# Optimization experiments

Hardware: AMD Instinct MI355X
Metric: run time of the kernel (lower is better)

## Reference

```python
import jax, jax.numpy as jnp
import numpy as np

VOCAB, EMBED, HIDDEN, LAYERS = 256, 256, 1024, 2
B, T = 128, 256


def gru_layer(x_seq, h0, W_ih, W_hh, b_ih, b_hh):
    """PyTorch-semantics GRU layer. x_seq:[B,T,in], h0:[B,H] -> ([B,T,H], [B,H]).
    n = tanh(W_in x + b_in + r * (W_hn h + b_hn)); h' = (1-z)*n + z*h.
    Input-gate GEMM is hoisted out of the scan (one big matmul over all T)."""
    H = h0.shape[-1]
    gi = jnp.einsum('bti,gi->btg', x_seq, W_ih) + b_ih  # [B,T,3H]
    gi = jnp.transpose(gi, (1, 0, 2))                   # [T,B,3H] scan over time

    def step(h, gi_t):
        gh = h @ W_hh.T + b_hh                          # [B,3H]
        i_r, i_z, i_n = jnp.split(gi_t, 3, axis=-1)
        h_r, h_z, h_n = jnp.split(gh, 3, axis=-1)
        r = jax.nn.sigmoid(i_r + h_r)
        z = jax.nn.sigmoid(i_z + h_z)
        n = jnp.tanh(i_n + r * h_n)
        h_new = (1.0 - z) * n + z * h
        return h_new, h_new

    h_last, ys = jax.lax.scan(step, h0, gi)
    return jnp.transpose(ys, (1, 0, 2)), h_last         # [B,T,H], [B,H]


def setup_inputs() -> dict:
    key = jax.random.key(0)
    ks = jax.random.split(key, 16)
    s = 1.0 / np.sqrt(HIDDEN)
    u = lambda k, shape: jax.random.uniform(k, shape, jnp.float32, -s, s)
    inp = {
        'x': jax.random.randint(ks[0], (B, T), 0, VOCAB),
        'h0': jax.random.normal(ks[1], (LAYERS, B, HIDDEN), jnp.float32),
        'emb': jax.random.normal(ks[2], (VOCAB, EMBED), jnp.float32),
        'W_ih0': u(ks[3], (3 * HIDDEN, EMBED)),
        'W_hh0': u(ks[4], (3 * HIDDEN, HIDDEN)),
        'b_ih0': u(ks[5], (3 * HIDDEN,)),
        'b_hh0': u(ks[6], (3 * HIDDEN,)),
        'W_ih1': u(ks[7], (3 * HIDDEN, HIDDEN)),
        'W_hh1': u(ks[8], (3 * HIDDEN, HIDDEN)),
        'b_ih1': u(ks[9], (3 * HIDDEN,)),
        'b_hh1': u(ks[10], (3 * HIDDEN,)),
        'fc_W': u(ks[11], (VOCAB, HIDDEN)),
        'fc_b': u(ks[12], (VOCAB,)),
    }
    return inp


def reference(x, h0, emb, W_ih0, W_hh0, b_ih0, b_hh0, W_ih1, W_hh1, b_ih1, b_hh1, fc_W, fc_b):
    xe = emb[x]                                          # [B,T,E]
    y0, h_last0 = gru_layer(xe, h0[0], W_ih0, W_hh0, b_ih0, b_hh0)
    y1, h_last1 = gru_layer(y0, h0[1], W_ih1, W_hh1, b_ih1, b_hh1)
    logits = y1[:, -1, :] @ fc_W.T + fc_b                # [B,VOCAB]
    h = jnp.stack([h_last0, h_last1], axis=0)            # [LAYERS,B,H]
    return logits, h
```

## Files before the change

kernel.cpp:

```cpp
#include <hip/hip_runtime.h>
#include <hip/hip_bf16.h>

using bf16x8 = __attribute__((ext_vector_type(8))) __bf16;
using short8 = __attribute__((ext_vector_type(8))) short;
using f32x4  = __attribute__((ext_vector_type(4))) float;
using f4     = __attribute__((ext_vector_type(4))) float;
using i32x4  = __attribute__((ext_vector_type(4))) int;

constexpr int NB = 128;
constexpr int NT = 256;
constexpr int NH = 1024;
constexpr int NE = 256;
constexpr int NV = 256;

constexpr int WHH_BYTES = 48 * 2048;
constexpr int GH_FLOATS = 24 * 256;
constexpr int NBLK = 256;

__device__ __forceinline__ void ldg_sc(i32x4& d, const void* p) {
  asm volatile("global_load_dwordx4 %0, %1, off sc0 sc1" : "=v"(d) : "v"(p));
}
__device__ __forceinline__ void stg_sc(void* p, i32x4 v) {
  asm volatile("global_store_dwordx4 %0, %1, off sc0 sc1" :: "v"(p), "v"(v) : "memory");
}
__device__ __forceinline__ void vm0_fence() {
  asm volatile("s_waitcnt vmcnt(0)" ::: "memory");
}
__device__ __forceinline__ void use_dep(i32x4& d) {
  asm volatile("" : "+v"(d));
}

__device__ __forceinline__ bf16x8 cvt8(const float* p) {
  short8 r;
  #pragma unroll
  for (int j = 0; j < 8; ++j)
    r[j] = (short)__bfloat16_as_ushort(__float2bfloat16(p[j]));
  return __builtin_bit_cast(bf16x8, r);
}

__global__ __launch_bounds__(256) void embcvt_kernel(const float* __restrict__ e,
                                                     __hip_bfloat16* __restrict__ o) {
  int i = blockIdx.x * 256 + threadIdx.x;
  o[i] = __float2bfloat16(e[i]);
}

template<int LAYER>
__global__ __launch_bounds__(384) void gru_kernel(
    const int* __restrict__ x,
    const __hip_bfloat16* __restrict__ embb,
    const float* __restrict__ Wih,
    const float* __restrict__ Whh,
    const float* __restrict__ bih,
    const float* __restrict__ bhh,
    const float* __restrict__ h0,
    const __hip_bfloat16* __restrict__ yin,
    __hip_bfloat16* __restrict__ yout,
    __hip_bfloat16* __restrict__ hbuf,
    float* __restrict__ hout,
    unsigned int* __restrict__ flags)
{
  extern __shared__ char smem[];
  char*  sWhh  = smem;
  float* sGh   = (float*)(smem + WHH_BYTES);
  float* sBias = sGh + GH_FLOATS;
  char*  sH    = (char*)(sBias + 64);

  const int tid  = threadIdx.x;
  const int lane = tid & 63;
  const int wv   = tid >> 6;
  const int mt   = wv & 1;
  const int ks   = wv >> 1;
  const int b    = blockIdx.x;
  const int rb   = (b >> 1) & 3;
  const int cidx = (b & 1) * 32 + (b >> 3);
  const int r0   = rb * 32;
  const int c0   = cidx * 16;
  unsigned int* pf = flags + rb * 64 * 16;
  const int slot = cidx;
  const int l16  = lane & 15;
  const int lk8  = (lane >> 4) * 8;

  for (int it = 0; it < 16; ++it) {
    int idx = it * 384 + tid;
    int gr = idx >> 7, kc = idx & 127;
    int grow = (gr >> 4) * NH + c0 + (gr & 15);
    short8 v = __builtin_bit_cast(short8, cvt8(Whh + grow * NH + kc * 8));
    *(short8*)(sWhh + ((gr * 2048 + kc * 16) ^ ((gr & 7) << 4))) = v;
  }
  if (tid < 16)       sBias[tid] = bih[c0 + tid] + bhh[c0 + tid];
  else if (tid < 32)  { int c = NH + c0 + tid - 16;   sBias[tid] = bih[c] + bhh[c]; }
  else if (tid < 48)  { int c = 2*NH + c0 + tid - 32; sBias[tid] = bih[c]; }
  else if (tid < 64)  { int c = 2*NH + c0 + tid - 48; sBias[tid] = bhh[c]; }

  constexpr int NFRAG = (LAYER == 0) ? 8 : 32;
  constexpr int KIN   = (LAYER == 0) ? NE : NH;
  bf16x8 wreg[NFRAG];
  #pragma unroll
  for (int kf = 0; kf < NFRAG; ++kf) {
    int grow = ks * NH + c0 + l16;
    wreg[kf] = cvt8(Wih + grow * KIN + kf * 32 + lk8);
  }

  float hown[2] = {0.f, 0.f};
  #pragma unroll
  for (int ei = 0; ei < 2; ++ei) {
    int e = tid + ei * 384;
    if (e < 512) {
      float hv = h0[(r0 + (e >> 4)) * NH + c0 + (e & 15)];
      hown[ei] = hv;
      ((unsigned short*)sH)[e] = __bfloat16_as_ushort(__float2bfloat16(hv));
    }
  }
  __syncthreads();
  if (tid < 64) {
    i32x4 hv = *(const i32x4*)(sH + (tid >> 1) * 32 + (tid & 1) * 16);
    stg_sc(hbuf + (r0 + (tid >> 1)) * NH + c0 + (tid & 1) * 8, hv);
    vm0_fence();
    if (tid == 0)
      __hip_atomic_store(pf + slot * 16, 1u, __ATOMIC_RELAXED,
                         __HIP_MEMORY_SCOPE_AGENT);
  }

  for (int t = 0; t < NT; ++t) {
    const __hip_bfloat16* rbuf = hbuf + (t & 1) * (NB * NH);
    __hip_bfloat16* wbuf = hbuf + ((t + 1) & 1) * (NB * NH);
    const int arow = r0 + mt * 16 + l16;
    const int bxor = (l16 & 7) << 4;
    float* abase = sGh + (lane >> 4) * 64 + l16;

    constexpr int P1 = (LAYER == 0) ? 4 : 24;
    f32x4 ai = {0.f, 0.f, 0.f, 0.f};
    const __hip_bfloat16* xptr;
    if constexpr (LAYER == 0) {
      int xid = x[arow * NT + t];
      xptr = embb + xid * NE + lk8;
    } else {
      xptr = yin + (arow * NT + t) * NH + lk8;
    }
    #pragma unroll
    for (int kk = 0; kk < P1; ++kk) {
      bf16x8 a = __builtin_bit_cast(bf16x8, *(const short8*)(xptr + kk * 32));
      ai = __builtin_amdgcn_mfma_f32_16x16x32_bf16(a, wreg[kk], ai, 0, 0, 0);
    }

    {
      unsigned int ep = (unsigned int)(t + 1);
      if (tid < 64) {
        const unsigned int* f = pf + tid * 16;
        while (__hip_atomic_load(f, __ATOMIC_RELAXED,
                                 __HIP_MEMORY_SCOPE_AGENT) < ep)
          __builtin_amdgcn_s_sleep(1);
      }
      __syncthreads();
    }

    const int nk = (ks < 2) ? 11 : 10;
    const __hip_bfloat16* aptr = rbuf + arow * NH + lk8;
    i32x4 fr[11];
    #pragma unroll
    for (int i = 0; i < 11; ++i)
      if (i < nk) ldg_sc(fr[i], aptr + (ks + 3 * i) * 32);

    #pragma unroll
    for (int kk = P1; kk < NFRAG; ++kk) {
      bf16x8 a = __builtin_bit_cast(bf16x8, *(const short8*)(xptr + kk * 32));
      ai = __builtin_amdgcn_mfma_f32_16x16x32_bf16(a, wreg[kk], ai, 0, 0, 0);
    }
    {
      float* p = abase + (18 + mt * 3 + ks) * 256;
      p[0] = ai[0]; p[16] = ai[1]; p[32] = ai[2]; p[48] = ai[3];
    }

    vm0_fence();
    #pragma unroll
    for (int i = 0; i < 11; ++i)
      if (i < nk) use_dep(fr[i]);
    {
      f32x4 ah0 = {0.f,0.f,0.f,0.f}, ah1 = {0.f,0.f,0.f,0.f}, ah2 = {0.f,0.f,0.f,0.f};
      const int bb0 = (l16)      * 2048 + lk8 * 2;
      const int bb1 = (16 + l16) * 2048 + lk8 * 2;
      const int bb2 = (32 + l16) * 2048 + lk8 * 2;
      #pragma unroll
      for (int i = 0; i < 11; ++i) {
        if (i < nk) {
          int kk = ks + 3 * i;
          bf16x8 a = __builtin_bit_cast(bf16x8, fr[i]);
          bf16x8 b0 = __builtin_bit_cast(bf16x8,
              *(const short8*)(sWhh + ((bb0 + kk * 64) ^ bxor)));
          ah0 = __builtin_amdgcn_mfma_f32_16x16x32_bf16(a, b0, ah0, 0, 0, 0);
          bf16x8 b1 = __builtin_bit_cast(bf16x8,
              *(const short8*)(sWhh + ((bb1 + kk * 64) ^ bxor)));
          ah1 = __builtin_amdgcn_mfma_f32_16x16x32_bf16(a, b1, ah1, 0, 0, 0);
          bf16x8 b2 = __builtin_bit_cast(bf16x8,
              *(const short8*)(sWhh + ((bb2 + kk * 64) ^ bxor)));
          ah2 = __builtin_amdgcn_mfma_f32_16x16x32_bf16(a, b2, ah2, 0, 0, 0);
        }
      }
      float* p0 = abase + (ks * 6 + mt * 3 + 0) * 256;
      float* p1 = abase + (ks * 6 + mt * 3 + 1) * 256;
      float* p2 = abase + (ks * 6 + mt * 3 + 2) * 256;
      p0[0] = ah0[0]; p0[16] = ah0[1]; p0[32] = ah0[2]; p0[48] = ah0[3];
      p1[0] = ah1[0]; p1[16] = ah1[1]; p1[32] = ah1[2]; p1[48] = ah1[3];
      p2[0] = ah2[0]; p2[16] = ah2[1]; p2[32] = ah2[2]; p2[48] = ah2[3];
    }
    __syncthreads();

    #pragma unroll
    for (int ei = 0; ei < 2; ++ei) {
      int e = tid + ei * 384;
      if (e < 512) {
        int lrow = e >> 4, lcol = e & 15;
        int m2 = lrow >> 4, off = (lrow & 15) * 16 + lcol;
        float ghr = sGh[(0*6 + m2*3 + 0) * 256 + off]
                  + sGh[(1*6 + m2*3 + 0) * 256 + off]
                  + sGh[(2*6 + m2*3 + 0) * 256 + off];
        float ghz = sGh[(0*6 + m2*3 + 1) * 256 + off]
                  + sGh[(1*6 + m2*3 + 1) * 256 + off]
                  + sGh[(2*6 + m2*3 + 1) * 256 + off];
        float ghn = sGh[(0*6 + m2*3 + 2) * 256 + off]
                  + sGh[(1*6 + m2*3 + 2) * 256 + off]
                  + sGh[(2*6 + m2*3 + 2) * 256 + off];
        float gir = sGh[(18 + m2*3 + 0) * 256 + off];
        float giz = sGh[(18 + m2*3 + 1) * 256 + off];
        float gin = sGh[(18 + m2*3 + 2) * 256 + off];
        float r = 1.f / (1.f + __expf(-(gir + ghr + sBias[lcol])));
        float z = 1.f / (1.f + __expf(-(giz + ghz + sBias[16 + lcol])));
        float npre = (gin + sBias[32 + lcol]) + r * (ghn + sBias[48 + lcol]);
        float n = 2.f / (1.f + __expf(-2.f * npre)) - 1.f;
        float hn = (1.f - z) * n + z * hown[ei];
        hown[ei] = hn;
        __hip_bfloat16 hb = __float2bfloat16(hn);
        ((unsigned short*)sH)[e] = __bfloat16_as_ushort(hb);
        if constexpr (LAYER == 0)
          yout[((r0 + lrow) * NT + t) * NH + c0 + lcol] = hb;
      }
    }

    __syncthreads();
    if (tid < 64) {
      i32x4 hv = *(const i32x4*)(sH + (tid >> 1) * 32 + (tid & 1) * 16);
      stg_sc(wbuf + (r0 + (tid >> 1)) * NH + c0 + (tid & 1) * 8, hv);
      vm0_fence();
      if (tid == 0)
        __hip_atomic_store(pf + slot * 16, (unsigned int)(t + 2),
                           __ATOMIC_RELAXED, __HIP_MEMORY_SCOPE_AGENT);
    }
  }

  #pragma unroll
  for (int ei = 0; ei < 2; ++ei) {
    int e = tid + ei * 384;
    if (e < 512) {
      int lrow = e >> 4, lcol = e & 15;
      hout[(r0 + lrow) * NH + c0 + lcol] = hown[ei];
    }
  }
}

__global__ __launch_bounds__(256) void logits_kernel(
    const __hip_bfloat16* __restrict__ h1,
    const float* __restrict__ fcW,
    const float* __restrict__ fcb,
    float* __restrict__ out)
{
  __shared__ float hrow[NH];
  int b = blockIdx.x, v = threadIdx.x;
  if (v < 128) {
    i32x4 hv;
    ldg_sc(hv, h1 + b * NH + v * 8);
    vm0_fence();
    use_dep(hv);
    short8 s = __builtin_bit_cast(short8, hv);
    #pragma unroll
    for (int j = 0; j < 8; ++j) {
      union { unsigned int i; float f; } c;
      c.i = ((unsigned int)(unsigned short)s[j]) << 16;
      hrow[v * 8 + j] = c.f;
    }
  }
  __syncthreads();
  float acc = fcb[v];
  for (int k = 0; k < NH; k += 4) {
    f4 wv = *(const f4*)(fcW + v * NH + k);
    #pragma unroll
    for (int j = 0; j < 4; ++j) acc += wv[j] * hrow[k + j];
  }
  out[b * NV + v] = acc;
}

extern "C" void kernel_launch(void* const* d_in, const int* in_sizes, int n_in,
                              void* d_out, int out_size, void* d_ws, size_t ws_size,
                              hipStream_t stream) {
  const int*   x    = (const int*)d_in[0];
  const float* h0   = (const float*)d_in[1];
  const float* emb  = (const float*)d_in[2];
  const float* Wih0 = (const float*)d_in[3];
  const float* Whh0 = (const float*)d_in[4];
  const float* bih0 = (const float*)d_in[5];
  const float* bhh0 = (const float*)d_in[6];
  const float* Wih1 = (const float*)d_in[7];
  const float* Whh1 = (const float*)d_in[8];
  const float* bih1 = (const float*)d_in[9];
  const float* bhh1 = (const float*)d_in[10];
  const float* fcW  = (const float*)d_in[11];
  const float* fcb  = (const float*)d_in[12];
  float* out = (float*)d_out;

  char* ws = (char*)d_ws;
  size_t off = 0;
  __hip_bfloat16* y0   = (__hip_bfloat16*)ws;            off += (size_t)NB * NT * NH * 2;
  __hip_bfloat16* hbuf = (__hip_bfloat16*)(ws + off);    off += (size_t)2 * NB * NH * 2;
  __hip_bfloat16* embb = (__hip_bfloat16*)(ws + off);    off += (size_t)NV * NE * 2;
  unsigned int*  flags0 = (unsigned int*)(ws + off);     off += 4 * 64 * 16 * 4;
  unsigned int*  flags1 = (unsigned int*)(ws + off);     off += 4 * 64 * 16 * 4;

  (void)hipMemsetAsync(flags0, 0, 2 * 4 * 64 * 16 * 4, stream);
  embcvt_kernel<<<dim3(NV * NE / 256), dim3(256), 0, stream>>>(emb, embb);

  constexpr int lds = WHH_BYTES + GH_FLOATS * 4 + 64 * 4 + 1024;
  (void)hipFuncSetAttribute(reinterpret_cast<const void*>(gru_kernel<0>),
                            hipFuncAttributeMaxDynamicSharedMemorySize, lds);
  (void)hipFuncSetAttribute(reinterpret_cast<const void*>(gru_kernel<1>),
                            hipFuncAttributeMaxDynamicSharedMemorySize, lds);

  gru_kernel<0><<<dim3(NBLK), dim3(384), lds, stream>>>(
      x, embb, Wih0, Whh0, bih0, bhh0, h0, y0, y0, hbuf, out + 32768, flags0);
  gru_kernel<1><<<dim3(NBLK), dim3(384), lds, stream>>>(
      x, embb, Wih1, Whh1, bih1, bhh1, h0 + NB * NH, y0, y0, hbuf,
      out + 32768 + NB * NH, flags1);
  logits_kernel<<<dim3(NB), dim3(256), 0, stream>>>(hbuf, fcW, fcb, out);
}
```

Before: 4.082 ms.

## Fuse both GRU layers into one wavefront-pipelined persistent kernel

```diff
diff --git a/kernel.cpp b/kernel.cpp
--- a/kernel.cpp
+++ b/kernel.cpp
@@ -12,10 +12,11 @@
 constexpr int NH = 1024;
 constexpr int NE = 256;
 constexpr int NV = 256;
+constexpr int BH = NB * NH;
 
 constexpr int WHH_BYTES = 48 * 2048;
-constexpr int GH_FLOATS = 24 * 256;
-constexpr int NBLK = 256;
+constexpr int NTILE     = 60;
+constexpr int GH_FLOATS = NTILE * 256;
 
 __device__ __forceinline__ void ldg_sc(i32x4& d, const void* p) {
   asm volatile("global_load_dwordx4 %0, %1, off sc0 sc1" : "=v"(d) : "v"(p));
@@ -44,18 +45,16 @@
   o[i] = __float2bfloat16(e[i]);
 }
 
-template<int LAYER>
-__global__ __launch_bounds__(384) void gru_kernel(
+__global__ __launch_bounds__(384, 2) void gru_fused(
     const int* __restrict__ x,
     const __hip_bfloat16* __restrict__ embb,
-    const float* __restrict__ Wih,
-    const float* __restrict__ Whh,
-    const float* __restrict__ bih,
-    const float* __restrict__ bhh,
+    const float* __restrict__ Wih0, const float* __restrict__ Whh0,
+    const float* __restrict__ bih0, const float* __restrict__ bhh0,
+    const float* __restrict__ Wih1, const float* __restrict__ Whh1,
+    const float* __restrict__ bih1, const float* __restrict__ bhh1,
     const float* __restrict__ h0,
-    const __hip_bfloat16* __restrict__ yin,
-    __hip_bfloat16* __restrict__ yout,
-    __hip_bfloat16* __restrict__ hbuf,
+    __hip_bfloat16* __restrict__ Ys,
+    __hip_bfloat16* __restrict__ hbuf1,
     float* __restrict__ hout,
     unsigned int* __restrict__ flags)
 {
@@ -65,24 +64,33 @@
   float* sBias = sGh + GH_FLOATS;
   char*  sH    = (char*)(sBias + 64);
 
-  const int tid  = threadIdx.x;
-  const int lane = tid & 63;
-  const int wv   = tid >> 6;
-  const int mt   = wv & 1;
-  const int ks   = wv >> 1;
-  const int b    = blockIdx.x;
-  const int rb   = (b >> 1) & 3;
-  const int cidx = (b & 1) * 32 + (b >> 3);
-  const int r0   = rb * 32;
-  const int c0   = cidx * 16;
-  unsigned int* pf = flags + rb * 64 * 16;
-  const int slot = cidx;
-  const int l16  = lane & 15;
-  const int lk8  = (lane >> 4) * 8;
+  const int tid   = threadIdx.x;
+  const int lane  = tid & 63;
+  const int wv    = tid >> 6;
+  const int mt    = wv & 1;
+  const int ks    = wv >> 1;
+  const int b     = blockIdx.x;
+  const int layer = b & 1;
+  const int idx   = b >> 1;
+  const int rb2   = idx & 1;
+  const int cidx  = idx >> 1;
+  const int r0    = rb2 * 64;
+  const int c0    = cidx * 16;
+  unsigned int* flagL  = flags + (layer * 2 + rb2) * 64 * 16;
+  unsigned int* flag0g = flags + (rb2) * 64 * 16;
+  const int l16 = lane & 15;
+  const int lk8 = (lane >> 4) * 8;
+
+  const float* Wih = layer ? Wih1 : Wih0;
+  const float* Whh = layer ? Whh1 : Whh0;
+  const float* bih = layer ? bih1 : bih0;
+  const float* bhh = layer ? bhh1 : bhh0;
+  const float* h0l = h0 + layer * BH;
+  float* houtl = hout + layer * BH;
 
   for (int it = 0; it < 16; ++it) {
-    int idx = it * 384 + tid;
-    int gr = idx >> 7, kc = idx & 127;
+    int id2 = it * 384 + tid;
+    int gr = id2 >> 7, kc = id2 & 127;
     int grow = (gr >> 4) * NH + c0 + (gr & 15);
     short8 v = __builtin_bit_cast(short8, cvt8(Whh + grow * NH + kc * 8));
     *(short8*)(sWhh + ((gr * 2048 + kc * 16) ^ ((gr & 7) << 4))) = v;
@@ -92,167 +100,261 @@
   else if (tid < 48)  { int c = 2*NH + c0 + tid - 32; sBias[tid] = bih[c]; }
   else if (tid < 64)  { int c = 2*NH + c0 + tid - 48; sBias[tid] = bhh[c]; }
 
-  constexpr int NFRAG = (LAYER == 0) ? 8 : 32;
-  constexpr int KIN   = (LAYER == 0) ? NE : NH;
-  bf16x8 wreg[NFRAG];
+  bf16x8 wreg[16];
+  if (layer == 0) {
+    #pragma unroll
+    for (int kf = 0; kf < 4; ++kf)
+      wreg[kf] = cvt8(Wih + (ks * NH + c0 + l16) * NE + mt * 128 + kf * 32 + lk8);
+  } else {
+    #pragma unroll
+    for (int kf = 0; kf < 16; ++kf)
+      wreg[kf] = cvt8(Wih + (ks * NH + c0 + l16) * NH + mt * 512 + kf * 32 + lk8);
+  }
+
+  float hown[3] = {0.f, 0.f, 0.f};
   #pragma unroll
-  for (int kf = 0; kf < NFRAG; ++kf) {
-    int grow = ks * NH + c0 + l16;
-    wreg[kf] = cvt8(Wih + grow * KIN + kf * 32 + lk8);
-  }
-
-  float hown[2] = {0.f, 0.f};
-  #pragma unroll
-  for (int ei = 0; ei < 2; ++ei) {
+  for (int ei = 0; ei < 3; ++ei) {
     int e = tid + ei * 384;
-    if (e < 512) {
-      float hv = h0[(r0 + (e >> 4)) * NH + c0 + (e & 15)];
+    if (e < 1024) {
+      int row = e >> 4, col = e & 15;
+      float hv = h0l[(r0 + row) * NH + c0 + col];
       hown[ei] = hv;
       ((unsigned short*)sH)[e] = __bfloat16_as_ushort(__float2bfloat16(hv));
     }
   }
   __syncthreads();
-  if (tid < 64) {
-    i32x4 hv = *(const i32x4*)(sH + (tid >> 1) * 32 + (tid & 1) * 16);
-    stg_sc(hbuf + (r0 + (tid >> 1)) * NH + c0 + (tid & 1) * 8, hv);
+  if (layer == 1) {
+    if (tid < 128) {
+      i32x4 hv = *(const i32x4*)(sH + (tid >> 1) * 32 + (tid & 1) * 16);
+      stg_sc(hbuf1 + (r0 + (tid >> 1)) * NH + c0 + (tid & 1) * 8, hv);
+    }
     vm0_fence();
     if (tid == 0)
-      __hip_atomic_store(pf + slot * 16, 1u, __ATOMIC_RELAXED,
+      __hip_atomic_store(flagL + cidx * 16, 1u, __ATOMIC_RELAXED,
                          __HIP_MEMORY_SCOPE_AGENT);
-  }
-
-  for (int t = 0; t < NT; ++t) {
-    const __hip_bfloat16* rbuf = hbuf + (t & 1) * (NB * NH);
-    __hip_bfloat16* wbuf = hbuf + ((t + 1) & 1) * (NB * NH);
-    const int arow = r0 + mt * 16 + l16;
-    const int bxor = (l16 & 7) << 4;
-    float* abase = sGh + (lane >> 4) * 64 + l16;
-
-    constexpr int P1 = (LAYER == 0) ? 4 : 24;
-    f32x4 ai = {0.f, 0.f, 0.f, 0.f};
-    const __hip_bfloat16* xptr;
-    if constexpr (LAYER == 0) {
-      int xid = x[arow * NT + t];
-      xptr = embb + xid * NE + lk8;
-    } else {
-      xptr = yin + (arow * NT + t) * NH + lk8;
-    }
-    #pragma unroll
-    for (int kk = 0; kk < P1; ++kk) {
-      bf16x8 a = __builtin_bit_cast(bf16x8, *(const short8*)(xptr + kk * 32));
-      ai = __builtin_amdgcn_mfma_f32_16x16x32_bf16(a, wreg[kk], ai, 0, 0, 0);
-    }
-
-    {
-      unsigned int ep = (unsigned int)(t + 1);
-      if (tid < 64) {
-        const unsigned int* f = pf + tid * 16;
+    __builtin_amdgcn_fence(__ATOMIC_ACQUIRE, "agent");
+  }
+
+  const int bxor = (l16 & 7) << 4;
+  float* abase = sGh + (lane >> 4) * 64 + l16;
+  const int nk = (ks < 2) ? 11 : 10;
+  const int bb0 = (l16)      * 2048 + lk8 * 2;
+  const int bb1 = (16 + l16) * 2048 + lk8 * 2;
+  const int bb2 = (32 + l16) * 2048 + lk8 * 2;
+
+  if (layer == 0) {
+    for (int t = 0; t < NT; ++t) {
+      #pragma unroll
+      for (int m4 = 0; m4 < 4; ++m4) {
+        int xid = x[(r0 + m4 * 16 + l16) * NT + t];
+        const __hip_bfloat16* xp = embb + xid * NE + mt * 128 + lk8;
+        f32x4 ii = {0.f, 0.f, 0.f, 0.f};
+        #pragma unroll
+        for (int kf = 0; kf < 4; ++kf) {
+          bf16x8 a = __builtin_bit_cast(bf16x8, *(const short8*)(xp + kf * 32));
+          ii = __builtin_amdgcn_mfma_f32_16x16x32_bf16(a, wreg[kf], ii, 0, 0, 0);
+        }
+        float* p = abase + (36 + (ks * 2 + mt) * 4 + m4) * 256;
+        p[0] = ii[0]; p[16] = ii[1]; p[32] = ii[2]; p[48] = ii[3];
+      }
+      if (t > 0 && tid < 64) {
+        unsigned int ep = (unsigned int)(t + 1);
+        const unsigned int* f = flagL + tid * 16;
         while (__hip_atomic_load(f, __ATOMIC_RELAXED,
                                  __HIP_MEMORY_SCOPE_AGENT) < ep)
           __builtin_amdgcn_s_sleep(1);
       }
       __syncthreads();
-    }
-
-    const int nk = (ks < 2) ? 11 : 10;
-    const __hip_bfloat16* aptr = rbuf + arow * NH + lk8;
-    i32x4 fr[11];
-    #pragma unroll
-    for (int i = 0; i < 11; ++i)
-      if (i < nk) ldg_sc(fr[i], aptr + (ks + 3 * i) * 32);
-
-    #pragma unroll
-    for (int kk = P1; kk < NFRAG; ++kk) {
-      bf16x8 a = __builtin_bit_cast(bf16x8, *(const short8*)(xptr + kk * 32));
-      ai = __builtin_amdgcn_mfma_f32_16x16x32_bf16(a, wreg[kk], ai, 0, 0, 0);
-    }
-    {
-      float* p = abase + (18 + mt * 3 + ks) * 256;
-      p[0] = ai[0]; p[16] = ai[1]; p[32] = ai[2]; p[48] = ai[3];
-    }
-
-    vm0_fence();
-    #pragma unroll
-    for (int i = 0; i < 11; ++i)
-      if (i < nk) use_dep(fr[i]);
-    {
-      f32x4 ah0 = {0.f,0.f,0.f,0.f}, ah1 = {0.f,0.f,0.f,0.f}, ah2 = {0.f,0.f,0.f,0.f};
-      const int bb0 = (l16)      * 2048 + lk8 * 2;
-      const int bb1 = (16 + l16) * 2048 + lk8 * 2;
-      const int bb2 = (32 + l16) * 2048 + lk8 * 2;
+      i32x4 fr0[11], fr1[11];
+      if (t == 0) {
+        #pragma unroll
+        for (int i = 0; i < 11; ++i)
+          if (i < nk) {
+            int kk = ks + 3 * i;
+            fr0[i] = __builtin_bit_cast(i32x4, cvt8(h0l + (r0 + mt*16 + l16) * NH + kk*32 + lk8));
+            fr1[i] = __builtin_bit_cast(i32x4, cvt8(h0l + (r0 + (2+mt)*16 + l16) * NH + kk*32 + lk8));
+          }
+      } else {
+        const __hip_bfloat16* ap0 = Ys + (size_t)(t-1) * BH + (r0 + mt*16 + l16) * NH + lk8;
+        const __hip_bfloat16* ap1 = Ys + (size_t)(t-1) * BH + (r0 + (2+mt)*16 + l16) * NH + lk8;
+        #pragma unroll
+        for (int i = 0; i < 11; ++i)
+          if (i < nk) { ldg_sc(fr0[i], ap0 + (ks + 3*i) * 32); ldg_sc(fr1[i], ap1 + (ks + 3*i) * 32); }
+        vm0_fence();
+        #pragma unroll
+        for (int i = 0; i < 11; ++i)
+          if (i < nk) { use_dep(fr0[i]); use_dep(fr1[i]); }
+      }
+      {
+        f32x4 a0g0={0,0,0,0}, a0g1={0,0,0,0}, a0g2={0,0,0,0};
+        f32x4 a1g0={0,0,0,0}, a1g1={0,0,0,0}, a1g2={0,0,0,0};
+        #pragma unroll
+        for (int i = 0; i < 11; ++i) {
+          if (i < nk) {
+            int kk = ks + 3 * i;
+            bf16x8 b0 = __builtin_bit_cast(bf16x8, *(const short8*)(sWhh + ((bb0 + kk*64) ^ bxor)));
+            bf16x8 b1 = __builtin_bit_cast(bf16x8, *(const short8*)(sWhh + ((bb1 + kk*64) ^ bxor)));
+            bf16x8 b2 = __builtin_bit_cast(bf16x8, *(const short8*)(sWhh + ((bb2 + kk*64) ^ bxor)));
+            bf16x8 a0 = __builtin_bit_cast(bf16x8, fr0[i]);
+            bf16x8 a1 = __builtin_bit_cast(bf16x8, fr1[i]);
+            a0g0 = __builtin_amdgcn_mfma_f32_16x16x32_bf16(a0, b0, a0g0, 0, 0, 0);
+            a0g1 = __builtin_amdgcn_mfma_f32_16x16x32_bf16(a0, b1, a0g1, 0, 0, 0);
+            a0g2 = __builtin_amdgcn_mfma_f32_16x16x32_bf16(a0, b2, a0g2, 0, 0, 0);
+            a1g0 = __builtin_amdgcn_mfma_f32_16x16x32_bf16(a1, b0, a1g0, 0, 0, 0);
+            a1g1 = __builtin_amdgcn_mfma_f32_16x16x32_bf16(a1, b1, a1g1, 0, 0, 0);
+            a1g2 = __builtin_amdgcn_mfma_f32_16x16x32_bf16(a1, b2, a1g2, 0, 0, 0);
+          }
+        }
+        float* p;
+        p = abase + ((ks*4 + mt)*3 + 0)*256;   p[0]=a0g0[0];p[16]=a0g0[1];p[32]=a0g0[2];p[48]=a0g0[3];
+        p = abase + ((ks*4 + mt)*3 + 1)*256;   p[0]=a0g1[0];p[16]=a0g1[1];p[32]=a0g1[2];p[48]=a0g1[3];
+        p = abase + ((ks*4 + mt)*3 + 2)*256;   p[0]=a0g2[0];p[16]=a0g2[1];p[32]=a0g2[2];p[48]=a0g2[3];
+        p = abase + ((ks*4 + 2+mt)*3 + 0)*256; p[0]=a1g0[0];p[16]=a1g0[1];p[32]=a1g0[2];p[48]=a1g0[3];
+        p = abase + ((ks*4 + 2+mt)*3 + 1)*256; p[0]=a1g1[0];p[16]=a1g1[1];p[32]=a1g1[2];p[48]=a1g1[3];
+        p = abase + ((ks*4 + 2+mt)*3 + 2)*256; p[0]=a1g2[0];p[16]=a1g2[1];p[32]=a1g2[2];p[48]=a1g2[3];
+      }
+      __syncthreads();
       #pragma unroll
-      for (int i = 0; i < 11; ++i) {
-        if (i < nk) {
-          int kk = ks + 3 * i;
-          bf16x8 a = __builtin_bit_cast(bf16x8, fr[i]);
-          bf16x8 b0 = __builtin_bit_cast(bf16x8,
-              *(const short8*)(sWhh + ((bb0 + kk * 64) ^ bxor)));
-          ah0 = __builtin_amdgcn_mfma_f32_16x16x32_bf16(a, b0, ah0, 0, 0, 0);
-          bf16x8 b1 = __builtin_bit_cast(bf16x8,
-              *(const short8*)(sWhh + ((bb1 + kk * 64) ^ bxor)));
-          ah1 = __builtin_amdgcn_mfma_f32_16x16x32_bf16(a, b1, ah1, 0, 0, 0);
-          bf16x8 b2 = __builtin_bit_cast(bf16x8,
-              *(const short8*)(sWhh + ((bb2 + kk * 64) ^ bxor)));
-          ah2 = __builtin_amdgcn_mfma_f32_16x16x32_bf16(a, b2, ah2, 0, 0, 0);
-        }
-      }
-      float* p0 = abase + (ks * 6 + mt * 3 + 0) * 256;
-      float* p1 = abase + (ks * 6 + mt * 3 + 1) * 256;
-      float* p2 = abase + (ks * 6 + mt * 3 + 2) * 256;
-      p0[0] = ah0[0]; p0[16] = ah0[1]; p0[32] = ah0[2]; p0[48] = ah0[3];
-      p1[0] = ah1[0]; p1[16] = ah1[1]; p1[32] = ah1[2]; p1[48] = ah1[3];
-      p2[0] = ah2[0]; p2[16] = ah2[1]; p2[32] = ah2[2]; p2[48] = ah2[3];
-    }
-    __syncthreads();
-
-    #pragma unroll
-    for (int ei = 0; ei < 2; ++ei) {
-      int e = tid + ei * 384;
-      if (e < 512) {
-        int lrow = e >> 4, lcol = e & 15;
-        int m2 = lrow >> 4, off = (lrow & 15) * 16 + lcol;
-        float ghr = sGh[(0*6 + m2*3 + 0) * 256 + off]
-                  + sGh[(1*6 + m2*3 + 0) * 256 + off]
-                  + sGh[(2*6 + m2*3 + 0) * 256 + off];
-        float ghz = sGh[(0*6 + m2*3 + 1) * 256 + off]
-                  + sGh[(1*6 + m2*3 + 1) * 256 + off]
-                  + sGh[(2*6 + m2*3 + 1) * 256 + off];
-        float ghn = sGh[(0*6 + m2*3 + 2) * 256 + off]
-                  + sGh[(1*6 + m2*3 + 2) * 256 + off]
-                  + sGh[(2*6 + m2*3 + 2) * 256 + off];
-        float gir = sGh[(18 + m2*3 + 0) * 256 + off];
-        float giz = sGh[(18 + m2*3 + 1) * 256 + off];
-        float gin = sGh[(18 + m2*3 + 2) * 256 + off];
-        float r = 1.f / (1.f + __expf(-(gir + ghr + sBias[lcol])));
-        float z = 1.f / (1.f + __expf(-(giz + ghz + sBias[16 + lcol])));
-        float npre = (gin + sBias[32 + lcol]) + r * (ghn + sBias[48 + lcol]);
-        float n = 2.f / (1.f + __expf(-2.f * npre)) - 1.f;
-        float hn = (1.f - z) * n + z * hown[ei];
-        hown[ei] = hn;
-        __hip_bfloat16 hb = __float2bfloat16(hn);
-        ((unsigned short*)sH)[e] = __bfloat16_as_ushort(hb);
-        if constexpr (LAYER == 0)
-          yout[((r0 + lrow) * NT + t) * NH + c0 + lcol] = hb;
-      }
-    }
-
-    __syncthreads();
-    if (tid < 64) {
-      i32x4 hv = *(const i32x4*)(sH + (tid >> 1) * 32 + (tid & 1) * 16);
-      stg_sc(wbuf + (r0 + (tid >> 1)) * NH + c0 + (tid & 1) * 8, hv);
+      for (int ei = 0; ei < 3; ++ei) {
+        int e = tid + ei * 384;
+        if (e < 1024) {
+          int lrow = e >> 4, lcol = e & 15;
+          int m4 = lrow >> 4, off = (lrow & 15) * 16 + lcol;
+          float ghr = sGh[((0*4+m4)*3+0)*256+off] + sGh[((1*4+m4)*3+0)*256+off] + sGh[((2*4+m4)*3+0)*256+off];
+          float ghz = sGh[((0*4+m4)*3+1)*256+off] + sGh[((1*4+m4)*3+1)*256+off] + sGh[((2*4+m4)*3+1)*256+off];
+          float ghn = sGh[((0*4+m4)*3+2)*256+off] + sGh[((1*4+m4)*3+2)*256+off] + sGh[((2*4+m4)*3+2)*256+off];
+          float gir = sGh[(36+0*4+m4)*256+off] + sGh[(36+1*4+m4)*256+off];
+          float giz = sGh[(36+2*4+m4)*256+off] + sGh[(36+3*4+m4)*256+off];
+          float gin = sGh[(36+4*4+m4)*256+off] + sGh[(36+5*4+m4)*256+off];
+          float r = 1.f / (1.f + __expf(-(gir + ghr + sBias[lcol])));
+          float z = 1.f / (1.f + __expf(-(giz + ghz + sBias[16 + lcol])));
+          float npre = (gin + sBias[32 + lcol]) + r * (ghn + sBias[48 + lcol]);
+          float n = 2.f / (1.f + __expf(-2.f * npre)) - 1.f;
+          float hn = (1.f - z) * n + z * hown[ei];
+          hown[ei] = hn;
+          ((unsigned short*)sH)[e] = __bfloat16_as_ushort(__float2bfloat16(hn));
+        }
+      }
+      __syncthreads();
+      if (tid < 128) {
+        i32x4 hv = *(const i32x4*)(sH + (tid >> 1) * 32 + (tid & 1) * 16);
+        stg_sc(Ys + (size_t)t * BH + (r0 + (tid >> 1)) * NH + c0 + (tid & 1) * 8, hv);
+      }
       vm0_fence();
       if (tid == 0)
-        __hip_atomic_store(pf + slot * 16, (unsigned int)(t + 2),
+        __hip_atomic_store(flagL + cidx * 16, (unsigned int)(t + 2),
                            __ATOMIC_RELAXED, __HIP_MEMORY_SCOPE_AGENT);
     }
+  } else {
+    for (int t = 0; t < NT; ++t) {
+      if (tid < 64) {
+        unsigned int ep = (unsigned int)(t + 1);
+        const unsigned int* f = flagL + tid * 16;
+        while (__hip_atomic_load(f, __ATOMIC_RELAXED,
+                                 __HIP_MEMORY_SCOPE_AGENT) < ep)
+          __builtin_amdgcn_s_sleep(1);
+      }
+      __syncthreads();
+      i32x4 fr0[11], fr1[11];
+      {
+        const __hip_bfloat16* ap0 = hbuf1 + (t & 1) * BH + (r0 + mt*16 + l16) * NH + lk8;
+        const __hip_bfloat16* ap1 = hbuf1 + (t & 1) * BH + (r0 + (2+mt)*16 + l16) * NH + lk8;
+        #pragma unroll
+        for (int i = 0; i < 11; ++i)
+          if (i < nk) { ldg_sc(fr0[i], ap0 + (ks + 3*i) * 32); ldg_sc(fr1[i], ap1 + (ks + 3*i) * 32); }
+      }
+      if (tid < 64) {
+        unsigned int ep = (unsigned int)(t + 2);
+        const unsigned int* f = flag0g + tid * 16;
+        while (__hip_atomic_load(f, __ATOMIC_RELAXED,
+                                 __HIP_MEMORY_SCOPE_AGENT) < ep)
+          __builtin_amdgcn_s_sleep(1);
+      }
+      __syncthreads();
+      #pragma unroll
+      for (int m4 = 0; m4 < 4; ++m4) {
+        const __hip_bfloat16* yp = Ys + (size_t)t * BH + (r0 + m4*16 + l16) * NH + mt * 512 + lk8;
+        f32x4 ii = {0.f, 0.f, 0.f, 0.f};
+        #pragma unroll
+        for (int kf = 0; kf < 16; ++kf) {
+          bf16x8 a = __builtin_bit_cast(bf16x8, *(const short8*)(yp + kf * 32));
+          ii = __builtin_amdgcn_mfma_f32_16x16x32_bf16(a, wreg[kf], ii, 0, 0, 0);
+        }
+        float* p = abase + (36 + (ks * 2 + mt) * 4 + m4) * 256;
+        p[0] = ii[0]; p[16] = ii[1]; p[32] = ii[2]; p[48] = ii[3];
+      }
+      vm0_fence();
+      #pragma unroll
+      for (int i = 0; i < 11; ++i)
+        if (i < nk) { use_dep(fr0[i]); use_dep(fr1[i]); }
+      {
+        f32x4 a0g0={0,0,0,0}, a0g1={0,0,0,0}, a0g2={0,0,0,0};
+        f32x4 a1g0={0,0,0,0}, a1g1={0,0,0,0}, a1g2={0,0,0,0};
+        #pragma unroll
+        for (int i = 0; i < 11; ++i) {
+          if (i < nk) {
+            int kk = ks + 3 * i;
+            bf16x8 b0 = __builtin_bit_cast(bf16x8, *(const short8*)(sWhh + ((bb0 + kk*64) ^ bxor)));
+            bf16x8 b1 = __builtin_bit_cast(bf16x8, *(const short8*)(sWhh + ((bb1 + kk*64) ^ bxor)));
+            bf16x8 b2 = __builtin_bit_cast(bf16x8, *(const short8*)(sWhh + ((bb2 + kk*64) ^ bxor)));
+            bf16x8 a0 = __builtin_bit_cast(bf16x8, fr0[i]);
+            bf16x8 a1 = __builtin_bit_cast(bf16x8, fr1[i]);
+            a0g0 = __builtin_amdgcn_mfma_f32_16x16x32_bf16(a0, b0, a0g0, 0, 0, 0);
+            a0g1 = __builtin_amdgcn_mfma_f32_16x16x32_bf16(a0, b1, a0g1, 0, 0, 0);
+            a0g2 = __builtin_amdgcn_mfma_f32_16x16x32_bf16(a0, b2, a0g2, 0, 0, 0);
+            a1g0 = __builtin_amdgcn_mfma_f32_16x16x32_bf16(a1, b0, a1g0, 0, 0, 0);
+            a1g1 = __builtin_amdgcn_mfma_f32_16x16x32_bf16(a1, b1, a1g1, 0, 0, 0);
+            a1g2 = __builtin_amdgcn_mfma_f32_16x16x32_bf16(a1, b2, a1g2, 0, 0, 0);
+          }
+        }
+        float* p;
+        p = abase + ((ks*4 + mt)*3 + 0)*256;   p[0]=a0g0[0];p[16]=a0g0[1];p[32]=a0g0[2];p[48]=a0g0[3];
+        p = abase + ((ks*4 + mt)*3 + 1)*256;   p[0]=a0g1[0];p[16]=a0g1[1];p[32]=a0g1[2];p[48]=a0g1[3];
+        p = abase + ((ks*4 + mt)*3 + 2)*256;   p[0]=a0g2[0];p[16]=a0g2[1];p[32]=a0g2[2];p[48]=a0g2[3];
+        p = abase + ((ks*4 + 2+mt)*3 + 0)*256; p[0]=a1g0[0];p[16]=a1g0[1];p[32]=a1g0[2];p[48]=a1g0[3];
+        p = abase + ((ks*4 + 2+mt)*3 + 1)*256; p[0]=a1g1[0];p[16]=a1g1[1];p[32]=a1g1[2];p[48]=a1g1[3];
+        p = abase + ((ks*4 + 2+mt)*3 + 2)*256; p[0]=a1g2[0];p[16]=a1g2[1];p[32]=a1g2[2];p[48]=a1g2[3];
+      }
+      __syncthreads();
+      #pragma unroll
+      for (int ei = 0; ei < 3; ++ei) {
+        int e = tid + ei * 384;
+        if (e < 1024) {
+          int lrow = e >> 4, lcol = e & 15;
+          int m4 = lrow >> 4, off = (lrow & 15) * 16 + lcol;
+          float ghr = sGh[((0*4+m4)*3+0)*256+off] + sGh[((1*4+m4)*3+0)*256+off] + sGh[((2*4+m4)*3+0)*256+off];
+          float ghz = sGh[((0*4+m4)*3+1)*256+off] + sGh[((1*4+m4)*3+1)*256+off] + sGh[((2*4+m4)*3+1)*256+off];
+          float ghn = sGh[((0*4+m4)*3+2)*256+off] + sGh[((1*4+m4)*3+2)*256+off] + sGh[((2*4+m4)*3+2)*256+off];
+          float gir = sGh[(36+0*4+m4)*256+off] + sGh[(36+1*4+m4)*256+off];
+          float giz = sGh[(36+2*4+m4)*256+off] + sGh[(36+3*4+m4)*256+off];
+          float gin = sGh[(36+4*4+m4)*256+off] + sGh[(36+5*4+m4)*256+off];
+          float r = 1.f / (1.f + __expf(-(gir + ghr + sBias[lcol])));
+          float z = 1.f / (1.f + __expf(-(giz + ghz + sBias[16 + lcol])));
+          float npre = (gin + sBias[32 + lcol]) + r * (ghn + sBias[48 + lcol]);
+          float n = 2.f / (1.f + __expf(-2.f * npre)) - 1.f;
+          float hn = (1.f - z) * n + z * hown[ei];
+          hown[ei] = hn;
+          ((unsigned short*)sH)[e] = __bfloat16_as_ushort(__float2bfloat16(hn));
+        }
+      }
+      __syncthreads();
+      if (tid < 128) {
+        i32x4 hv = *(const i32x4*)(sH + (tid >> 1) * 32 + (tid & 1) * 16);
+        stg_sc(hbuf1 + ((t + 1) & 1) * BH + (r0 + (tid >> 1)) * NH + c0 + (tid & 1) * 8, hv);
+      }
+      vm0_fence();
+      if (tid == 0)
+        __hip_atomic_store(flagL + cidx * 16, (unsigned int)(t + 2),
+                           __ATOMIC_RELAXED, __HIP_MEMORY_SCOPE_AGENT);
+    }
   }
 
   #pragma unroll
-  for (int ei = 0; ei < 2; ++ei) {
+  for (int ei = 0; ei < 3; ++ei) {
     int e = tid + ei * 384;
-    if (e < 512) {
-      int lrow = e >> 4, lcol = e & 15;
-      hout[(r0 + lrow) * NH + c0 + lcol] = hown[ei];
+    if (e < 1024) {
+      int row = e >> 4, col = e & 15;
+      houtl[(r0 + row) * NH + c0 + col] = hown[ei];
     }
   }
 }
@@ -308,25 +410,20 @@
 
   char* ws = (char*)d_ws;
   size_t off = 0;
-  __hip_bfloat16* y0   = (__hip_bfloat16*)ws;            off += (size_t)NB * NT * NH * 2;
-  __hip_bfloat16* hbuf = (__hip_bfloat16*)(ws + off);    off += (size_t)2 * NB * NH * 2;
-  __hip_bfloat16* embb = (__hip_bfloat16*)(ws + off);    off += (size_t)NV * NE * 2;
-  unsigned int*  flags0 = (unsigned int*)(ws + off);     off += 4 * 64 * 16 * 4;
-  unsigned int*  flags1 = (unsigned int*)(ws + off);     off += 4 * 64 * 16 * 4;
-
-  (void)hipMemsetAsync(flags0, 0, 2 * 4 * 64 * 16 * 4, stream);
+  __hip_bfloat16* Ys    = (__hip_bfloat16*)ws;           off += (size_t)NT * BH * 2;
+  __hip_bfloat16* hbuf1 = (__hip_bfloat16*)(ws + off);   off += (size_t)2 * BH * 2;
+  __hip_bfloat16* embb  = (__hip_bfloat16*)(ws + off);   off += (size_t)NV * NE * 2;
+  unsigned int*   flags = (unsigned int*)(ws + off);     off += 2 * 2 * 64 * 16 * 4;
+
+  (void)hipMemsetAsync(flags, 0, 2 * 2 * 64 * 16 * 4, stream);
   embcvt_kernel<<<dim3(NV * NE / 256), dim3(256), 0, stream>>>(emb, embb);
 
-  constexpr int lds = WHH_BYTES + GH_FLOATS * 4 + 64 * 4 + 1024;
-  (void)hipFuncSetAttribute(reinterpret_cast<const void*>(gru_kernel<0>),
+  constexpr int lds = WHH_BYTES + GH_FLOATS * 4 + 64 * 4 + 2048;
+  (void)hipFuncSetAttribute(reinterpret_cast<const void*>(gru_fused),
                             hipFuncAttributeMaxDynamicSharedMemorySize, lds);
-  (void)hipFuncSetAttribute(reinterpret_cast<const void*>(gru_kernel<1>),
-                            hipFuncAttributeMaxDynamicSharedMemorySize, lds);
-
-  gru_kernel<0><<<dim3(NBLK), dim3(384), lds, stream>>>(
-      x, embb, Wih0, Whh0, bih0, bhh0, h0, y0, y0, hbuf, out + 32768, flags0);
-  gru_kernel<1><<<dim3(NBLK), dim3(384), lds, stream>>>(
-      x, embb, Wih1, Whh1, bih1, bhh1, h0 + NB * NH, y0, y0, hbuf,
-      out + 32768 + NB * NH, flags1);
-  logits_kernel<<<dim3(NB), dim3(256), 0, stream>>>(hbuf, fcW, fcb, out);
-}
+
+  gru_fused<<<dim3(256), dim3(384), lds, stream>>>(
+      x, embb, Wih0, Whh0, bih0, bhh0, Wih1, Whh1, bih1, bhh1,
+      h0, Ys, hbuf1, out + 32768, flags);
+  logits_kernel<<<dim3(NB), dim3(256), 0, stream>>>(hbuf1, fcW, fcb, out);
+}
```

Result: slower. 5.561 ms (+36.2%).
